# Kernel optimization log

Measured on AMD Instinct MI355X. Metric: run time of the kernel, lower is better.

## Reference

```python
import jax, jax.numpy as jnp
import numpy as np

SEQ = 4096
D = 1024      # input_dim
DK = 1024     # query_dim
DV = 1024     # encoding_dim
STD = 0.02


def setup_inputs() -> dict:
    key = jax.random.key(0)
    kz, kq, kk, kv = jax.random.split(key, 4)
    z = jax.random.normal(kz, (SEQ, D), dtype=jnp.float32)
    # weights stored as [in, out], matching q = z @ Wq
    Wq = STD * jax.random.normal(kq, (D, DK), dtype=jnp.float32)
    Wk = STD * jax.random.normal(kk, (D, DK), dtype=jnp.float32)
    Wv = STD * jax.random.normal(kv, (D, DV), dtype=jnp.float32)
    return {"z": z, "Wq": Wq, "Wk": Wk, "Wv": Wv}


def reference(z, Wq, Wk, Wv):
    q = z @ Wq                      # [S, dk]
    k = z @ Wk                      # [S, dk]
    v = z @ Wv                      # [S, dv]
    # NOTE: original applies the 1/sqrt(dk) scale AFTER softmax (to the probabilities)
    attn = jax.nn.softmax(q @ k.T, axis=-1) * (DK ** -0.5)  # [S, S]
    return attn @ v                 # [S, dv]
```

## Files before the change

### kernel.cpp

```cpp
#include <hip/hip_runtime.h>

typedef unsigned short u16;
typedef unsigned int u32;
typedef __attribute__((ext_vector_type(8))) short bf16x8;
typedef __attribute__((ext_vector_type(8))) _Float16 f16x8;
typedef __attribute__((ext_vector_type(4))) float f32x4;

__device__ inline u16 f2bf(float f){
  union { float f; unsigned u; } v; v.f = f;
  unsigned r = v.u + 0x7FFFu + ((v.u >> 16) & 1u);
  return (u16)(r >> 16);
}
__device__ inline float bf2f(u16 u){
  union { unsigned u; float f; } v; v.u = ((unsigned)u) << 16;
  return v.f;
}
__device__ inline u16 f2h(float f){
  union { _Float16 h; u16 u; } v; v.h = (_Float16)f; return v.u;
}

__device__ inline void gload16(const u16* g, u16* l){
  __builtin_amdgcn_global_load_lds(
      (const __attribute__((address_space(1))) u32*)(const void*)g,
      (__attribute__((address_space(3))) u32*)(void*)l, 16, 0, 0);
}

#define WAITV(n) asm volatile("s_waitcnt vmcnt(" #n ")" ::: "memory")
#define FENCE()  asm volatile("" ::: "memory")

__global__ __launch_bounds__(256) void split_wqk(const float* __restrict__ wq,
                                                 const float* __restrict__ wk,
                                                 u16* __restrict__ qh, u16* __restrict__ ql,
                                                 u16* __restrict__ kh, u16* __restrict__ kl){
  int b = blockIdx.x;
  const float* x; u16 *hi, *lo;
  int i;
  if (b < 1024){ x = wq; hi = qh; lo = ql; i = b * 256 + threadIdx.x; }
  else         { x = wk; hi = kh; lo = kl; i = (b - 1024) * 256 + threadIdx.x; }
  float4 v = ((const float4*)x)[i];
  float a0 = v.x, a1 = v.y, a2 = v.z, a3 = v.w;
  u16 h0 = f2bf(a0), h1 = f2bf(a1), h2 = f2bf(a2), h3 = f2bf(a3);
  ushort4 h; h.x = h0; h.y = h1; h.z = h2; h.w = h3;
  ushort4 l; l.x = f2bf(a0 - bf2f(h0)); l.y = f2bf(a1 - bf2f(h1));
  l.z = f2bf(a2 - bf2f(h2)); l.w = f2bf(a3 - bf2f(h3));
  ((ushort4*)hi)[i] = h;
  ((ushort4*)lo)[i] = l;
}

__global__ __launch_bounds__(256) void conv_h16(const float* __restrict__ x,
                                                u16* __restrict__ h16, int n4){
  int i = blockIdx.x * 256 + threadIdx.x;
  if (i >= n4) return;
  float4 v = ((const float4*)x)[i];
  ushort4 g; g.x = f2h(v.x); g.y = f2h(v.y); g.z = f2h(v.z); g.w = f2h(v.w);
  ((ushort4*)h16)[i] = g;
}

__global__ __launch_bounds__(256) void transpose_wv16(
    const float* __restrict__ W, u16* __restrict__ H){
  __shared__ float t[64][65];
  int d0 = blockIdx.y * 64, n0 = blockIdx.x * 64;
  int tid = threadIdx.x;
  int r = tid >> 4, c4 = (tid & 15) * 4;
  for (int rr = r; rr < 64; rr += 16){
    float4 v = *(const float4*)&W[(size_t)(d0 + rr) * 1024 + n0 + c4];
    t[rr][c4 + 0] = v.x; t[rr][c4 + 1] = v.y; t[rr][c4 + 2] = v.z; t[rr][c4 + 3] = v.w;
  }
  __syncthreads();
  int n = tid >> 4, d4 = (tid & 15) * 4;
  for (int nn = n; nn < 64; nn += 16){
    ushort4 h;
    h.x = f2h(t[d4 + 0][nn]); h.y = f2h(t[d4 + 1][nn]);
    h.z = f2h(t[d4 + 2][nn]); h.w = f2h(t[d4 + 3][nn]);
    *(ushort4*)&H[(size_t)(n0 + nn) * 1024 + d0 + d4] = h;
  }
}

template<int IN, int EPI>
__global__ __launch_bounds__(256) void gemm_bt(
    const u16* __restrict__ Ah, const u16* __restrict__ Al, int lda,
    const u16* __restrict__ Bh, const u16* __restrict__ Bl, int ldb,
    void* __restrict__ C0, int ldc, int K, size_t zslab){
  constexpr int NPL = 4;
  constexpr int DEPTH = 1;
  constexpr int NBUF = DEPTH + 1;
  __shared__ __align__(16) u16 sm[NBUF * NPL * 4096];

  const int kz = blockIdx.z * K;
  Ah += kz; Bh += kz; Al += kz; Bl += kz;

  const int tid = threadIdx.x;
  const int lane = tid & 63, wave = tid >> 6;
  const int wr = wave >> 1, wc = wave & 1;
  const int lr = lane & 15, kg = lane >> 4;

  const int nwg = gridDim.x * gridDim.y;
  const int id = blockIdx.y * gridDim.x + blockIdx.x;
  const int chunk = nwg >> 3;
  const int swz = (id & 7) * chunk + (id >> 3);
  const int bx = swz % gridDim.x, by = swz / gridDim.x;
  const int m0 = by * 128, n0 = bx * 128;

  const int l_r = lane >> 2, l_c = lane & 3;
  const int st_chunk = l_c ^ ((l_r + (l_r >> 2)) & 3);
  const int rd_swz = (lr + (lr >> 2)) & 3;

  f32x4 acc[4][4];
  #pragma unroll
  for (int m = 0; m < 4; m++)
    #pragma unroll
    for (int n = 0; n < 4; n++)
      acc[m][n] = (f32x4){0.f, 0.f, 0.f, 0.f};

  auto STAGE = [&](int buf, int k0){
    #pragma unroll
    for (int c = 0; c < NPL * 2; ++c){
      int pc = c * 4 + wave;
      int p = pc >> 3, ch = pc & 7;
      const u16* g = (p == 0) ? Ah : (p == 1) ? Al : (p == 2) ? Bh : Bl;
      int ld = (p < 2) ? lda : ldb;
      int rb = (p < 2) ? m0 : n0;
      int r = ch * 16 + l_r;
      const u16* src = g + (size_t)(rb + r) * ld + k0 + st_chunk * 8;
      u16* dst = &sm[((size_t)buf * NPL + p) * 4096 + ch * 512];
      gload16(src, dst);
    }
  };

  const int KT = K >> 5;
  STAGE(0, 0);

  int bufc = 0, pfb = DEPTH % NBUF;
  for (int kt = 0; kt < KT; ++kt){
    const int pf = kt + DEPTH;
    if (pf < KT){
      STAGE(pfb, pf * 32);
      WAITV(8);
    } else {
      WAITV(0);
    }
    __builtin_amdgcn_s_barrier();
    FENCE();

    const u16* pA  = &sm[((size_t)bufc * NPL + 0) * 4096];
    const u16* pAl = &sm[((size_t)bufc * NPL + 1) * 4096];
    const u16* pB  = &sm[((size_t)bufc * NPL + 2) * 4096];
    const u16* pBl = &sm[((size_t)bufc * NPL + 3) * 4096];

    const int slot = (kg ^ rd_swz) * 8;
    bf16x8 afh[4], bfh[4], afl[4], bfl[4];
    #pragma unroll
    for (int m = 0; m < 4; m++){
      int r = wr * 64 + m * 16 + lr;
      afh[m] = *(const bf16x8*)&pA[r * 32 + slot];
      afl[m] = *(const bf16x8*)&pAl[r * 32 + slot];
    }
    #pragma unroll
    for (int n = 0; n < 4; n++){
      int r = wc * 64 + n * 16 + lr;
      bfh[n] = *(const bf16x8*)&pB[r * 32 + slot];
      bfl[n] = *(const bf16x8*)&pBl[r * 32 + slot];
    }
    #pragma unroll
    for (int m = 0; m < 4; m++)
      #pragma unroll
      for (int n = 0; n < 4; n++){
        acc[m][n] = __builtin_amdgcn_mfma_f32_16x16x32_bf16(afh[m], bfh[n], acc[m][n], 0, 0, 0);
        acc[m][n] = __builtin_amdgcn_mfma_f32_16x16x32_bf16(afl[m], bfh[n], acc[m][n], 0, 0, 0);
        acc[m][n] = __builtin_amdgcn_mfma_f32_16x16x32_bf16(afh[m], bfl[n], acc[m][n], 0, 0, 0);
      }
    FENCE();
    __builtin_amdgcn_s_barrier();
    bufc = (bufc + 1 == NBUF) ? 0 : bufc + 1;
    pfb  = (pfb  + 1 == NBUF) ? 0 : pfb  + 1;
  }

  const int row0 = m0 + wr * 64, col0 = n0 + wc * 64 + lr;
  float* C = (float*)C0 + (size_t)blockIdx.z * zslab;
  #pragma unroll
  for (int m = 0; m < 4; m++)
    #pragma unroll
    for (int n = 0; n < 4; n++)
      #pragma unroll
      for (int r = 0; r < 4; r++){
        int row = row0 + m * 16 + kg * 4 + r;
        int col = col0 + n * 16;
        C[(size_t)row * ldc + col] = acc[m][n][r];
      }
}

__global__ __launch_bounds__(256) void gemm_dual(
    const u16* __restrict__ A0, int lda0, const u16* __restrict__ B0, int ldb0,
    u16* __restrict__ C0_, int ldc0, int gx0,
    const u16* __restrict__ A1, int lda1, const u16* __restrict__ B1, int ldb1,
    u16* __restrict__ C1_, int ldc1, int gx1, int K){
  constexpr int NPL = 2, DEPTH = 2, NBUF = 3;
  __shared__ __align__(16) u16 sm[NBUF * NPL * 4096];

  const int id = blockIdx.x;
  const int l = id & 255;
  const int swz = (l & 7) * 32 + (l >> 3);
  const u16* Ah; const u16* Bh; u16* C; int lda, ldb, ldc, gx;
  if (id < 256){ Ah = A0; Bh = B0; C = C0_; lda = lda0; ldb = ldb0; ldc = ldc0; gx = gx0; }
  else         { Ah = A1; Bh = B1; C = C1_; lda = lda1; ldb = ldb1; ldc = ldc1; gx = gx1; }
  const int bx = swz % gx, by = swz / gx;
  const int m0 = by * 128, n0 = bx * 128;

  const int tid = threadIdx.x;
  const int lane = tid & 63, wave = tid >> 6;
  const int wr = wave >> 1, wc = wave & 1;
  const int lr = lane & 15, kg = lane >> 4;
  const int l_r = lane >> 2, l_c = lane & 3;
  const int st_chunk = l_c ^ ((l_r + (l_r >> 2)) & 3);
  const int rd_swz = (lr + (lr >> 2)) & 3;

  f32x4 acc[4][4];
  #pragma unroll
  for (int m = 0; m < 4; m++)
    #pragma unroll
    for (int n = 0; n < 4; n++)
      acc[m][n] = (f32x4){0.f, 0.f, 0.f, 0.f};

  auto STAGE = [&](int buf, int k0){
    #pragma unroll
    for (int c = 0; c < NPL * 2; ++c){
      int pc = c * 4 + wave;
      int p = pc >> 3, ch = pc & 7;
      const u16* g = (p == 0) ? Ah : Bh;
      int ld = (p == 0) ? lda : ldb;
      int rb = (p == 0) ? m0 : n0;
      int r = ch * 16 + l_r;
      const u16* src = g + (size_t)(rb + r) * ld + k0 + st_chunk * 8;
      u16* dst = &sm[((size_t)buf * NPL + p) * 4096 + ch * 512];
      gload16(src, dst);
    }
  };

  const int KT = K >> 5;
  STAGE(0, 0);
  if (KT > 1) STAGE(1, 32);

  int bufc = 0, pfb = DEPTH % NBUF;
  for (int kt = 0; kt < KT; ++kt){
    const int pf = kt + DEPTH;
    if (pf < KT){
      STAGE(pfb, pf * 32);
      WAITV(8);
    } else if (kt + 1 < KT){
      WAITV(4);
    } else {
      WAITV(0);
    }
    __builtin_amdgcn_s_barrier();
    FENCE();

    const u16* pA = &sm[((size_t)bufc * NPL + 0) * 4096];
    const u16* pB = &sm[((size_t)bufc * NPL + 1) * 4096];

    const int slot = (kg ^ rd_swz) * 8;
    f16x8 ah[4], bh[4];
    #pragma unroll
    for (int m = 0; m < 4; m++){
      int r = wr * 64 + m * 16 + lr;
      ah[m] = *(const f16x8*)&pA[r * 32 + slot];
    }
    #pragma unroll
    for (int n = 0; n < 4; n++){
      int r = wc * 64 + n * 16 + lr;
      bh[n] = *(const f16x8*)&pB[r * 32 + slot];
    }
    #pragma unroll
    for (int m = 0; m < 4; m++)
      #pragma unroll
      for (int n = 0; n < 4; n++)
        acc[m][n] = __builtin_amdgcn_mfma_f32_16x16x32_f16(ah[m], bh[n], acc[m][n], 0, 0, 0);
    FENCE();
    __builtin_amdgcn_s_barrier();
    bufc = (bufc + 1 == NBUF) ? 0 : bufc + 1;
    pfb  = (pfb  + 1 == NBUF) ? 0 : pfb  + 1;
  }

  const int row0 = m0 + wr * 64, col0 = n0 + wc * 64 + lr;
  #pragma unroll
  for (int m = 0; m < 4; m++)
    #pragma unroll
    for (int n = 0; n < 4; n++)
      #pragma unroll
      for (int r = 0; r < 4; r++){
        int row = row0 + m * 16 + kg * 4 + r;
        int col = col0 + n * 16;
        C[(size_t)row * ldc + col] = f2h(acc[m][n][r]);
      }
}

template<int EPI>
__global__ __launch_bounds__(512, 1) void gemm256(
    const u16* __restrict__ A, int lda,
    const u16* __restrict__ B, int ldb,
    void* __restrict__ C0z, int l0, void* __restrict__ C1z, int l1,
    void* __restrict__ C2z, int l2, void* __restrict__ C3z, int l3,
    int K){
  __shared__ __align__(16) u16 sm[2 * 32768];

  const int tid = threadIdx.x;
  const int lane = tid & 63, wave = tid >> 6;
  const int wr = wave >> 2, wc = wave & 3;
  const int lr = lane & 15, kg = lane >> 4;
  const int g7 = lr & 7;

  const int nwg = gridDim.x * gridDim.y;
  const int id = blockIdx.y * gridDim.x + blockIdx.x;
  const int chunk = nwg >> 3;
  const int swz = (id & 7) * chunk + (id >> 3);
  const int bx = swz % gridDim.x, by = swz / gridDim.x;
  const int m0 = by * 256, n0 = bx * 256;

  A += (size_t)blockIdx.z * (size_t)K;
  B += (size_t)blockIdx.z * (size_t)K;
  void* Cp; int ldc;
  if (blockIdx.z == 0){ Cp = C0z; ldc = l0; }
  else if (blockIdx.z == 1){ Cp = C1z; ldc = l1; }
  else if (blockIdx.z == 2){ Cp = C2z; ldc = l2; }
  else { Cp = C3z; ldc = l3; }

  auto STAGE = [&](int buf, int k0){
    #pragma unroll
    for (int rd = 0; rd < 8; ++rd){
      int p = rd >> 2;
      int r0 = (rd & 3) * 64 + wave * 8;
      const u16* g = p ? B : A;
      int ld = p ? ldb : lda;
      int rb = p ? n0 : m0;
      int grow = rb + r0 + (lane >> 3);
      int gch = (lane & 7) ^ (lane >> 3);
      const u16* src = g + (size_t)grow * ld + k0 + gch * 8;
      u16* dst = &sm[(size_t)buf * 32768 + p * 16384 + r0 * 64];
      gload16(src, dst);
    }
  };

  f32x4 acc[8][4];
  #pragma unroll
  for (int m = 0; m < 8; m++)
    #pragma unroll
    for (int n = 0; n < 4; n++)
      acc[m][n] = (f32x4){0.f, 0.f, 0.f, 0.f};

  const int KT = K >> 6;
  STAGE(0, 0);

  int bufc = 0;
  for (int kt = 0; kt < KT; ++kt){
    WAITV(0);
    __builtin_amdgcn_s_barrier();
    FENCE();
    if (kt + 1 < KT) STAGE(bufc ^ 1, (kt + 1) * 64);

    const u16* pA = &sm[(size_t)bufc * 32768];
    const u16* pB = pA + 16384;
    #pragma unroll
    for (int ks = 0; ks < 2; ++ks){
      f16x8 b[4], a[8];
      #pragma unroll
      for (int n = 0; n < 4; n++){
        int R = wc * 64 + n * 16 + lr;
        b[n] = *(const f16x8*)&pB[R * 64 + (((ks * 4 + kg) ^ g7) * 8)];
      }
      #pragma unroll
      for (int m = 0; m < 8; m++){
        int R = wr * 128 + m * 16 + lr;
        a[m] = *(const f16x8*)&pA[R * 64 + (((ks * 4 + kg) ^ g7) * 8)];
      }
      __builtin_amdgcn_s_setprio(1);
      #pragma unroll
      for (int m = 0; m < 8; m++)
        #pragma unroll
        for (int n = 0; n < 4; n++)
          acc[m][n] = __builtin_amdgcn_mfma_f32_16x16x32_f16(a[m], b[n], acc[m][n], 0, 0, 0);
      __builtin_amdgcn_s_setprio(0);
    }
    FENCE();
    bufc ^= 1;
  }

  const int row0 = m0 + wr * 128, col0 = n0 + wc * 64 + lr;
  #pragma unroll
  for (int m = 0; m < 8; m++)
    #pragma unroll
    for (int n = 0; n < 4; n++)
      #pragma unroll
      for (int r = 0; r < 4; r++){
        int row = row0 + m * 16 + kg * 4 + r;
        int col = col0 + n * 16;
        if (EPI == 0) ((float*)Cp)[(size_t)row * ldc + col] = acc[m][n][r];
        else          ((u16*)Cp)[(size_t)row * ldc + col] = f2h(acc[m][n][r]);
      }
}

__global__ __launch_bounds__(256) void reduce_t(u16* __restrict__ dst,
                                                const float* __restrict__ s0,
                                                const float* __restrict__ s1,
                                                const float* __restrict__ s2,
                                                const float* __restrict__ s3){
  int idx = blockIdx.x * 256 + threadIdx.x;
  float4 a = ((const float4*)s0)[idx];
  float4 b = ((const float4*)s1)[idx];
  float4 c = ((const float4*)s2)[idx];
  float4 d = ((const float4*)s3)[idx];
  ushort4 o;
  o.x = f2h((a.x + b.x) + (c.x + d.x));
  o.y = f2h((a.y + b.y) + (c.y + d.y));
  o.z = f2h((a.z + b.z) + (c.z + d.z));
  o.w = f2h((a.w + b.w) + (c.w + d.w));
  ((ushort4*)dst)[idx] = o;
}

__global__ __launch_bounds__(256) void reduce_pv4(float* __restrict__ out,
                                                  const float* __restrict__ s1,
                                                  const float* __restrict__ s2,
                                                  const float* __restrict__ s3){
  int idx = blockIdx.x * 256 + threadIdx.x;
  float4 a = ((const float4*)out)[idx];
  float4 b = ((const float4*)s1)[idx];
  float4 c = ((const float4*)s2)[idx];
  float4 d = ((const float4*)s3)[idx];
  float4 o;
  o.x = (a.x + b.x) + (c.x + d.x);
  o.y = (a.y + b.y) + (c.y + d.y);
  o.z = (a.z + b.z) + (c.z + d.z);
  o.w = (a.w + b.w) + (c.w + d.w);
  ((float4*)out)[idx] = o;
}

__global__ __launch_bounds__(256) void softmax16(u16* __restrict__ S){
  int row = blockIdx.x;
  _Float16* srow = (_Float16*)(S + (size_t)row * 4096);
  __shared__ float e[4096];
  __shared__ float red[4];
  int tid = threadIdx.x;

  float m = -1e30f;
  for (int i = tid * 8; i < 4096; i += 2048){
    f16x8 v = *(const f16x8*)(srow + i);
    #pragma unroll
    for (int j = 0; j < 8; j++) m = fmaxf(m, (float)v[j]);
  }
  for (int o = 32; o > 0; o >>= 1) m = fmaxf(m, __shfl_xor(m, o));
  if ((tid & 63) == 0) red[tid >> 6] = m;
  __syncthreads();
  m = fmaxf(fmaxf(red[0], red[1]), fmaxf(red[2], red[3]));

  float s = 0.f;
  for (int i = tid * 8; i < 4096; i += 2048){
    f16x8 v = *(const f16x8*)(srow + i);
    #pragma unroll
    for (int j = 0; j < 8; j++){
      float ev = __expf((float)v[j] - m);
      s += ev;
      e[i + j] = ev;
    }
  }
  for (int o = 32; o > 0; o >>= 1) s += __shfl_xor(s, o);
  __syncthreads();
  if ((tid & 63) == 0) red[tid >> 6] = s;
  __syncthreads();
  s = (red[0] + red[1]) + (red[2] + red[3]);

  float scale = 0.03125f / s;
  for (int i = tid * 8; i < 4096; i += 2048){
    f16x8 o;
    #pragma unroll
    for (int j = 0; j < 8; j++) o[j] = (_Float16)(e[i + j] * scale);
    *(f16x8*)(srow + i) = o;
  }
}

extern "C" void kernel_launch(void* const* d_in, const int* in_sizes, int n_in,
                              void* d_out, int out_size, void* d_ws, size_t ws_size,
                              hipStream_t stream){
  const float* z  = (const float*)d_in[0];
  const float* Wq = (const float*)d_in[1];
  const float* Wk = (const float*)d_in[2];
  const float* Wv = (const float*)d_in[3];
  char* ws = (char*)d_ws;
  const size_t MB = 1ull << 20;

  u16* t16   = (u16*)(ws + 0 * MB);
  u16* z16   = (u16*)(ws + 8 * MB);
  u16* vt16  = (u16*)(ws + 16 * MB);
  u16* S16   = (u16*)(ws + 24 * MB);
  u16* m16   = (u16*)(ws + 88 * MB);
  float* pv1 = (float*)(ws + 56 * MB);
  float* pv2 = (float*)(ws + 72 * MB);
  float* pv3 = (float*)(ws + 0 * MB);
  u16* wqh   = (u16*)(ws + 24 * MB);
  u16* wql   = (u16*)(ws + 26 * MB);
  u16* wkh   = (u16*)(ws + 28 * MB);
  u16* wkl   = (u16*)(ws + 30 * MB);
  u16* wvt16 = (u16*)(ws + 32 * MB);
  float* msl = (float*)(ws + 40 * MB);

  conv_h16<<<4096, 256, 0, stream>>>(z, z16, 4096 * 1024 / 4);
  split_wqk<<<2048, 256, 0, stream>>>(Wq, Wk, wqh, wql, wkh, wkl);
  transpose_wv16<<<dim3(16, 16), 256, 0, stream>>>(Wv, wvt16);

  gemm_bt<0, 0><<<dim3(8, 8, 4), 256, 0, stream>>>(wkh, wkl, 1024,
      wqh, wql, 1024, msl, 1024, 256, (size_t)1024 * 1024);
  reduce_t<<<1024, 256, 0, stream>>>(m16, msl, msl + 1048576,
      msl + 2097152, msl + 3145728);

  gemm_dual<<<512, 256, 0, stream>>>(
      z16, 1024, m16, 1024, t16, 1024, 8,
      wvt16, 1024, z16, 1024, vt16, 4096, 32, 1024);

  gemm256<1><<<dim3(16, 16, 1), 512, 0, stream>>>(t16, 1024, z16, 1024,
      S16, 4096, S16, 4096, S16, 4096, S16, 4096, 1024);

  softmax16<<<4096, 256, 0, stream>>>(S16);

  gemm256<0><<<dim3(4, 16, 4), 512, 0, stream>>>(S16, 4096, vt16, 4096,
      (float*)d_out, 1024, pv1, 1024, pv2, 1024, pv3, 1024, 1024);

  reduce_pv4<<<4096, 256, 0, stream>>>((float*)d_out, pv1, pv2, pv3);
}
```

Measured before the change: 158.5 us.

## Restructure 256x256 GEMM into quarter-tile ping-pong pipeline with split LDS halves

Replaces the simple double-buffered 256x256 fp16 GEMM main loop with an eight-phase schedule. A and B tiles are split into halves, and each wave computes quadrant sub-tiles in turn. Each phase issues one async global-to-LDS half-tile load while MFMAs run on already-read registers, with barriers and lgkmcnt waits around every phase. The aim is to hide global-load latency and LDS reads behind MFMA work, at the cost of many more barriers and more complex buffer indexing. This is the HipKittens-style 8-wave ping-pong pattern.

Measured after the change: 158.9 us. About the same (+0.2%).

```diff
diff --git a/kernel.cpp b/kernel.cpp
--- a/kernel.cpp
+++ b/kernel.cpp
@@ -27,6 +27,9 @@
 
 #define WAITV(n) asm volatile("s_waitcnt vmcnt(" #n ")" ::: "memory")
 #define FENCE()  asm volatile("" ::: "memory")
+#define BARR     __builtin_amdgcn_s_barrier()
+#define MSYNC    do{ asm volatile("s_waitcnt lgkmcnt(0)" ::: "memory"); \
+                     __builtin_amdgcn_sched_barrier(0); }while(0)
 
 __global__ __launch_bounds__(256) void split_wqk(const float* __restrict__ wq,
                                                  const float* __restrict__ wk,
@@ -139,7 +142,7 @@
     } else {
       WAITV(0);
     }
-    __builtin_amdgcn_s_barrier();
+    BARR;
     FENCE();
 
     const u16* pA  = &sm[((size_t)bufc * NPL + 0) * 4096];
@@ -170,7 +173,7 @@
         acc[m][n] = __builtin_amdgcn_mfma_f32_16x16x32_bf16(afh[m], bfl[n], acc[m][n], 0, 0, 0);
       }
     FENCE();
-    __builtin_amdgcn_s_barrier();
+    BARR;
     bufc = (bufc + 1 == NBUF) ? 0 : bufc + 1;
     pfb  = (pfb  + 1 == NBUF) ? 0 : pfb  + 1;
   }
@@ -251,7 +254,7 @@
     } else {
       WAITV(0);
     }
-    __builtin_amdgcn_s_barrier();
+    BARR;
     FENCE();
 
     const u16* pA = &sm[((size_t)bufc * NPL + 0) * 4096];
@@ -275,7 +278,7 @@
       for (int n = 0; n < 4; n++)
         acc[m][n] = __builtin_amdgcn_mfma_f32_16x16x32_f16(ah[m], bh[n], acc[m][n], 0, 0, 0);
     FENCE();
-    __builtin_amdgcn_s_barrier();
+    BARR;
     bufc = (bufc + 1 == NBUF) ? 0 : bufc + 1;
     pfb  = (pfb  + 1 == NBUF) ? 0 : pfb  + 1;
   }
@@ -294,19 +297,18 @@
 }
 
 template<int EPI>
-__global__ __launch_bounds__(512, 1) void gemm256(
+__global__ __launch_bounds__(512, 1) void gemm256p(
     const u16* __restrict__ A, int lda,
     const u16* __restrict__ B, int ldb,
     void* __restrict__ C0z, int l0, void* __restrict__ C1z, int l1,
     void* __restrict__ C2z, int l2, void* __restrict__ C3z, int l3,
     int K){
-  __shared__ __align__(16) u16 sm[2 * 32768];
+  __shared__ __align__(16) u16 sm[8 * 8192];
 
   const int tid = threadIdx.x;
   const int lane = tid & 63, wave = tid >> 6;
   const int wr = wave >> 2, wc = wave & 3;
   const int lr = lane & 15, kg = lane >> 4;
-  const int g7 = lr & 7;
 
   const int nwg = gridDim.x * gridDim.y;
   const int id = blockIdx.y * gridDim.x + blockIdx.x;
@@ -323,20 +325,34 @@
   else if (blockIdx.z == 2){ Cp = C2z; ldc = l2; }
   else { Cp = C3z; ldc = l3; }
 
-  auto STAGE = [&](int buf, int k0){
-    #pragma unroll
-    for (int rd = 0; rd < 8; ++rd){
-      int p = rd >> 2;
-      int r0 = (rd & 3) * 64 + wave * 8;
-      const u16* g = p ? B : A;
-      int ld = p ? ldb : lda;
-      int rb = p ? n0 : m0;
-      int grow = rb + r0 + (lane >> 3);
-      int gch = (lane & 7) ^ (lane >> 3);
-      const u16* src = g + (size_t)grow * ld + k0 + gch * 8;
-      u16* dst = &sm[(size_t)buf * 32768 + p * 16384 + r0 * 64];
-      gload16(src, dst);
-    }
+  auto SH = [&](int op, int buf, int half, int k0){
+    u16* base = &sm[(size_t)((op * 2 + buf) * 2 + half) * 8192];
+    const u16* g = op ? B : A;
+    const int ld = op ? ldb : lda;
+    const int rb = op ? n0 : m0;
+    #pragma unroll
+    for (int rd = 0; rd < 2; ++rd){
+      int ri = rd * 64 + wave * 8 + (lane >> 3);
+      int r  = op ? ((ri >> 5) * 64 + half * 32 + (ri & 31))
+                  : ((ri >> 6) * 128 + half * 64 + (ri & 63));
+      int gch = (lane & 7) ^ (ri & 7);
+      gload16(g + (size_t)(rb + r) * ld + k0 + gch * 8,
+              base + ri * 64 + (lane & 7) * 8);
+    }
+  };
+
+  const u16* pA0h0 = sm + 0 * 8192;  const u16* pA0h1 = sm + 1 * 8192;
+  const u16* pA1h0 = sm + 2 * 8192;  const u16* pA1h1 = sm + 3 * 8192;
+  const u16* pB0h0 = sm + 4 * 8192;  const u16* pB0h1 = sm + 5 * 8192;
+  const u16* pB1h0 = sm + 6 * 8192;  const u16* pB1h1 = sm + 7 * 8192;
+
+  auto RA = [&](const u16* h, int m, int ks) -> f16x8 {
+    int ri = wr * 64 + m * 16 + lr;
+    return *(const f16x8*)&h[ri * 64 + (((ks * 4 + kg) ^ (ri & 7)) * 8)];
+  };
+  auto RB = [&](const u16* h, int n, int ks) -> f16x8 {
+    int ri = wc * 32 + n * 16 + lr;
+    return *(const f16x8*)&h[ri * 64 + (((ks * 4 + kg) ^ (ri & 7)) * 8)];
   };
 
   f32x4 acc[8][4];
@@ -346,42 +362,60 @@
     for (int n = 0; n < 4; n++)
       acc[m][n] = (f32x4){0.f, 0.f, 0.f, 0.f};
 
+  f16x8 a[4][2], b0[2][2], b1[2][2];
+
+#define RDA(H) do{ _Pragma("unroll") \
+    for (int m_ = 0; m_ < 4; m_++){ a[m_][0] = RA(H, m_, 0); a[m_][1] = RA(H, m_, 1); } }while(0)
+#define RDB(DST, H) do{ _Pragma("unroll") \
+    for (int n_ = 0; n_ < 2; n_++){ DST[n_][0] = RB(H, n_, 0); DST[n_][1] = RB(H, n_, 1); } }while(0)
+#define MMQ(QM, QN, BB) do{ \
+    __builtin_amdgcn_s_setprio(1); \
+    _Pragma("unroll") \
+    for (int m_ = 0; m_ < 4; m_++){ \
+      _Pragma("unroll") \
+      for (int n_ = 0; n_ < 2; n_++){ \
+        acc[QM*4+m_][QN*2+n_] = __builtin_amdgcn_mfma_f32_16x16x32_f16(a[m_][0], BB[n_][0], acc[QM*4+m_][QN*2+n_], 0, 0, 0); \
+        acc[QM*4+m_][QN*2+n_] = __builtin_amdgcn_mfma_f32_16x16x32_f16(a[m_][1], BB[n_][1], acc[QM*4+m_][QN*2+n_], 0, 0, 0); \
+      } } \
+    __builtin_amdgcn_s_setprio(0); }while(0)
+
   const int KT = K >> 6;
-  STAGE(0, 0);
-
-  int bufc = 0;
-  for (int kt = 0; kt < KT; ++kt){
-    WAITV(0);
-    __builtin_amdgcn_s_barrier();
-    FENCE();
-    if (kt + 1 < KT) STAGE(bufc ^ 1, (kt + 1) * 64);
-
-    const u16* pA = &sm[(size_t)bufc * 32768];
-    const u16* pB = pA + 16384;
-    #pragma unroll
-    for (int ks = 0; ks < 2; ++ks){
-      f16x8 b[4], a[8];
-      #pragma unroll
-      for (int n = 0; n < 4; n++){
-        int R = wc * 64 + n * 16 + lr;
-        b[n] = *(const f16x8*)&pB[R * 64 + (((ks * 4 + kg) ^ g7) * 8)];
-      }
-      #pragma unroll
-      for (int m = 0; m < 8; m++){
-        int R = wr * 128 + m * 16 + lr;
-        a[m] = *(const f16x8*)&pA[R * 64 + (((ks * 4 + kg) ^ g7) * 8)];
-      }
-      __builtin_amdgcn_s_setprio(1);
-      #pragma unroll
-      for (int m = 0; m < 8; m++)
-        #pragma unroll
-        for (int n = 0; n < 4; n++)
-          acc[m][n] = __builtin_amdgcn_mfma_f32_16x16x32_f16(a[m], b[n], acc[m][n], 0, 0, 0);
-      __builtin_amdgcn_s_setprio(0);
-    }
-    FENCE();
-    bufc ^= 1;
-  }
+  SH(0, 0, 0, 0); SH(0, 0, 1, 0); SH(1, 0, 0, 0); SH(1, 0, 1, 0);
+  SH(0, 1, 0, 64); SH(1, 1, 0, 64); SH(1, 1, 1, 64);
+  WAITV(6);
+  BARR;
+
+  for (int j = 0; j < (KT >> 1); ++j){
+    const int T = 2 * j;
+    const bool s2 = (T + 2) < KT;
+    const int k1 = (T + 1) * 64, k2 = (T + 2) * 64, k3 = (T + 3) * 64;
+
+    RDA(pA0h0); RDB(b0, pB0h0);
+    SH(0, 1, 1, k1);
+    BARR; MSYNC; MMQ(0, 0, b0); BARR;
+    RDB(b1, pB0h1);
+    if (s2) SH(0, 0, 0, k2);
+    BARR; MSYNC; MMQ(0, 1, b1); BARR;
+    RDA(pA0h1);
+    if (s2) SH(1, 0, 0, k2);
+    BARR; MSYNC; MMQ(1, 0, b0); BARR;
+    if (s2){ SH(1, 0, 1, k2); WAITV(6); } else { WAITV(0); }
+    BARR; MSYNC; MMQ(1, 1, b1); BARR;
+    RDA(pA1h0); RDB(b0, pB1h0);
+    if (s2) SH(0, 0, 1, k2);
+    BARR; MSYNC; MMQ(0, 0, b0); BARR;
+    RDB(b1, pB1h1);
+    if (s2) SH(0, 1, 0, k3);
+    BARR; MSYNC; MMQ(0, 1, b1); BARR;
+    RDA(pA1h1);
+    if (s2) SH(1, 1, 0, k3);
+    BARR; MSYNC; MMQ(1, 0, b0); BARR;
+    if (s2){ SH(1, 1, 1, k3); WAITV(6); } else { WAITV(0); }
+    BARR; MSYNC; MMQ(1, 1, b1); BARR;
+  }
+#undef RDA
+#undef RDB
+#undef MMQ
 
   const int row0 = m0 + wr * 128, col0 = n0 + wc * 64 + lr;
   #pragma unroll
@@ -513,12 +547,12 @@
       z16, 1024, m16, 1024, t16, 1024, 8,
       wvt16, 1024, z16, 1024, vt16, 4096, 32, 1024);
 
-  gemm256<1><<<dim3(16, 16, 1), 512, 0, stream>>>(t16, 1024, z16, 1024,
+  gemm256p<1><<<dim3(16, 16, 1), 512, 0, stream>>>(t16, 1024, z16, 1024,
       S16, 4096, S16, 4096, S16, 4096, S16, 4096, 1024);
 
   softmax16<<<4096, 256, 0, stream>>>(S16);
 
-  gemm256<0><<<dim3(4, 16, 4), 512, 0, stream>>>(S16, 4096, vt16, 4096,
+  gemm256p<0><<<dim3(4, 16, 4), 512, 0, stream>>>(S16, 4096, vt16, 4096,
       (float*)d_out, 1024, pv1, 1024, pv2, 1024, pv3, 1024, 1024);
 
   reduce_pv4<<<4096, 256, 0, stream>>>((float*)d_out, pv1, pv2, pv3);
```
